# Kernel tuning notes

Measured on AMD Instinct MI355X. Metric: run time of the kernel, lower is better.

## Reference

```python
import jax, jax.numpy as jnp
import numpy as np

NPOINT = 2048
RADII = (0.4, 0.8)
NSAMPLES = (16, 32)
EPS = 1e-5


def _fps(xyz, npoint):
    # iterative farthest point sampling, start at index 0 (matches CUDA kernel)
    B, N, _ = xyz.shape

    def step(carry, _):
        dist, last = carry  # dist [B,N], last [B]
        lx = jnp.take_along_axis(xyz, last[:, None, None], axis=1)  # [B,1,3]
        d = jnp.sum((xyz - lx) ** 2, axis=-1)  # [B,N]
        dist = jnp.minimum(dist, d)
        nxt = jnp.argmax(dist, axis=1).astype(jnp.int32)
        return (dist, nxt), last

    init = (jnp.full((B, N), 1e10, xyz.dtype), jnp.zeros((B,), jnp.int32))
    _, idxs = jax.lax.scan(step, init, None, length=npoint)
    return idxs.T  # [B, npoint]


def _ball_query(radius, nsample, xyz, new_xyz):
    # first-nsample points within radius, in original order; pad with first hit (0 if none)
    N = xyz.shape[1]
    d2 = jnp.sum((new_xyz[:, :, None, :] - xyz[:, None, :, :]) ** 2, axis=-1)  # [B,S,N]
    mask = d2 < radius * radius
    ar = jnp.arange(N, dtype=jnp.int32)
    key = jnp.where(mask, ar, N + ar)  # in-range first, stable original order
    order = jnp.argsort(key, axis=-1)[..., :nsample].astype(jnp.int32)  # [B,S,ns]
    cnt = mask.sum(axis=-1, keepdims=True)  # [B,S,1]
    valid = jnp.arange(nsample) < cnt
    return jnp.where(valid, order, order[..., :1])


def _bn_relu(x):
    # training-mode BatchNorm (gamma=1, beta=0) over all dims but channel (last)
    red = tuple(range(x.ndim - 1))
    mu = x.mean(axis=red, keepdims=True)
    var = x.var(axis=red, keepdims=True)
    return jax.nn.relu((x - mu) * jax.lax.rsqrt(var + EPS))


def _scale(xyz, new_xyz, feats, radius, nsample, ws):
    idx = _ball_query(radius, nsample, xyz, new_xyz)  # [B,S,ns]
    B, S, ns = idx.shape
    flat = idx.reshape(B, S * ns)
    gx = jnp.take_along_axis(xyz, flat[..., None], axis=1).reshape(B, S, ns, 3)
    gx = gx - new_xyz[:, :, None, :]  # relative coords
    gf = jnp.take_along_axis(feats, flat[..., None], axis=1).reshape(B, S, ns, -1)
    h = jnp.concatenate([gx, gf], axis=-1)  # [B,S,ns,3+C]
    for w in ws:
        h = _bn_relu(h @ w)  # pointwise conv (kernel 1) + BN + ReLU
    return h.max(axis=2)  # max-pool over group -> [B,S,Cout]


def setup_inputs() -> dict:
    key = jax.random.key(0)
    ks = jax.random.split(key, 16)
    s = 0.02
    return {
        "xyz": jax.random.normal(ks[0], (8, 8192, 3), jnp.float32),
        "features": jax.random.normal(ks[1], (8, 8192, 64), jnp.float32),
        "w0_0": jax.random.normal(ks[2], (67, 64), jnp.float32) * s,
        "w0_1": jax.random.normal(ks[3], (64, 64), jnp.float32) * s,
        "w0_2": jax.random.normal(ks[4], (64, 128), jnp.float32) * s,
        "w1_0": jax.random.normal(ks[5], (67, 64), jnp.float32) * s,
        "w1_1": jax.random.normal(ks[6], (64, 64), jnp.float32) * s,
        "w1_2": jax.random.normal(ks[7], (64, 128), jnp.float32) * s,
        "agg_w": jax.random.normal(ks[8], (256, 256), jnp.float32) * s,
        "agg_b": jax.random.normal(ks[9], (256,), jnp.float32) * s,
        "conf_w": jax.random.normal(ks[10], (256, 256), jnp.float32) * s,
        "cls_w": jax.random.normal(ks[11], (256, 3), jnp.float32) * s,
        "cls_b": jax.random.normal(ks[12], (3,), jnp.float32) * s,
    }


def reference(xyz, features, w0_0, w0_1, w0_2, w1_0, w1_1, w1_2,
              agg_w, agg_b, conf_w, cls_w, cls_b):
    idx = _fps(xyz, NPOINT)  # [B,S]
    new_xyz = jnp.take_along_axis(xyz, idx[..., None], axis=1)  # [B,S,3]
    f0 = _scale(xyz, new_xyz, features, RADII[0], NSAMPLES[0], (w0_0, w0_1, w0_2))
    f1 = _scale(xyz, new_xyz, features, RADII[1], NSAMPLES[1], (w1_0, w1_1, w1_2))
    h = jnp.concatenate([f0, f1], axis=-1)  # [B,S,256]
    h = _bn_relu(h @ agg_w + agg_b)  # aggregation Linear + BN + ReLU
    c = _bn_relu(h @ conf_w)  # confidence hidden layer
    cls = c @ cls_w + cls_b  # [B,S,num_class]
    return new_xyz, h, cls
```

## Files before the change

### kernel.cpp

```cpp
#include <hip/hip_runtime.h>
#include <cstdint>
#include <cstddef>

constexpr int Bb = 8;
constexpr int Nn = 8192;
constexpr int Ss = 2048;
constexpr int BS = Bb * Ss;

typedef float vfloat2 __attribute__((ext_vector_type(2)));

__global__ __launch_bounds__(1024) void fps_kernel(const float* __restrict__ xyz,
                                                   float* __restrict__ new_xyz) {
  __shared__ float lx[Nn * 3];
  __shared__ int sidx[Ss];
  __shared__ float rv32[2][16];
  __shared__ double rv64[2][16];
  __shared__ int ri[2][16];
  const int b = blockIdx.x;
  const int tid = threadIdx.x;
  const float* xb = xyz + (size_t)b * Nn * 3;
  for (int e = tid; e < Nn * 3; e += 1024) lx[e] = xb[e];
  __syncthreads();
  vfloat2 px2[4], py2[4], pz2[4], df2[4];
  double dist[8];
#pragma unroll
  for (int jj = 0; jj < 4; ++jj) {
    const int p0 = tid + (2 * jj) * 1024, p1 = tid + (2 * jj + 1) * 1024;
    px2[jj] = (vfloat2){lx[p0 * 3 + 0], lx[p1 * 3 + 0]};
    py2[jj] = (vfloat2){lx[p0 * 3 + 1], lx[p1 * 3 + 1]};
    pz2[jj] = (vfloat2){lx[p0 * 3 + 2], lx[p1 * 3 + 2]};
    df2[jj] = (vfloat2){3.0e38f, 3.0e38f};
    dist[2 * jj] = 1e10;
    dist[2 * jj + 1] = 1e10;
  }
  const int lane = tid & 63, wid = tid >> 6;
  int cur = 0;
  double lv = -1.0;
  int li = tid;
  float wv32_c = -1.0f;
  double wv64_c = -1.0;
  int wi_c = 0;
  for (int i = 0; i < Ss; ++i) {
    if (tid == 0) sidx[i] = cur;
    const float cxf = lx[cur * 3 + 0], cyf = lx[cur * 3 + 1], czf = lx[cur * 3 + 2];
    const vfloat2 cx2 = {cxf, cxf}, cy2 = {cyf, cyf}, cz2 = {czf, czf};
    unsigned need = 0;
#pragma unroll
    for (int jj = 0; jj < 4; ++jj) {
      const vfloat2 dx = px2[jj] - cx2;
      const vfloat2 dy = py2[jj] - cy2;
      const vfloat2 dz = pz2[jj] - cz2;
      const vfloat2 d2 = dx * dx + dy * dy + dz * dz;
      need |= (d2.x <= df2[jj].x) ? (1u << (2 * jj)) : 0u;
      need |= (d2.y <= df2[jj].y) ? (1u << (2 * jj + 1)) : 0u;
    }
    bool changed = false;
    if (need) {
#pragma unroll
      for (int j = 0; j < 8; ++j) {
        if (need & (1u << j)) {
          const float pxs = px2[j >> 1][j & 1];
          const float pys = py2[j >> 1][j & 1];
          const float pzs = pz2[j >> 1][j & 1];
          double dx = __dsub_rn((double)pxs, (double)cxf);
          double dy = __dsub_rn((double)pys, (double)cyf);
          double dz = __dsub_rn((double)pzs, (double)czf);
          double d = __dadd_rn(__dadd_rn(__dmul_rn(dx, dx), __dmul_rn(dy, dy)),
                               __dmul_rn(dz, dz));
          if (d < dist[j]) {
            dist[j] = d;
            const float dfn = (float)d * 1.000002f;
            if (j & 1) df2[j >> 1].y = dfn; else df2[j >> 1].x = dfn;
            changed = true;
          }
        }
      }
    }
    const unsigned long long anyb = __ballot(changed);
    if (changed) {
      lv = -1.0;
      li = 0;
#pragma unroll
      for (int j = 0; j < 8; ++j) {
        if (dist[j] > lv) { lv = dist[j]; li = tid + j * 1024; }
      }
    }
    if (anyb) {
      const float lv32 = (float)lv;
      float m32 = lv32;
#pragma unroll
      for (int off = 1; off < 64; off <<= 1) m32 = fmaxf(m32, __shfl_xor(m32, off));
      const unsigned long long em = __ballot(lv32 == m32);
      if (__popcll(em) == 1) {
        const int w = (int)__builtin_ctzll(em);
        wi_c = __shfl(li, w);
        wv64_c = __shfl(lv, w);
        wv32_c = m32;
      } else {
        double bv = lv;
        int bi = li;
#pragma unroll
        for (int off = 1; off < 64; off <<= 1) {
          double ov = __shfl_xor(bv, off);
          int oi = __shfl_xor(bi, off);
          if (ov > bv || (ov == bv && oi < bi)) { bv = ov; bi = oi; }
        }
        wv64_c = bv;
        wi_c = bi;
        wv32_c = (float)bv;
      }
    }
    const int pb = i & 1;
    if (lane == 0) { rv32[pb][wid] = wv32_c; rv64[pb][wid] = wv64_c; ri[pb][wid] = wi_c; }
    __syncthreads();
    const float mine = rv32[pb][lane & 15];
    float g32 = mine;
#pragma unroll
    for (int off = 1; off < 16; off <<= 1) g32 = fmaxf(g32, __shfl_xor(g32, off));
    const unsigned long long bm = __ballot((lane < 16) && (mine == g32));
    if (__popcll(bm) == 1) {
      cur = ri[pb][(int)__builtin_ctzll(bm)];
    } else {
      double gv = -1.0;
      int gi = 0x7fffffff;
      unsigned mm = (unsigned)bm;
      while (mm) {
        const int w = (int)__builtin_ctz(mm);
        mm &= mm - 1;
        const double ov = rv64[pb][w];
        const int oi = ri[pb][w];
        if (ov > gv || (ov == gv && oi < gi)) { gv = ov; gi = oi; }
      }
      cur = gi;
    }
  }
  __syncthreads();
  float* nxb = new_xyz + (size_t)b * Ss * 3;
  for (int e = tid; e < Ss * 3; e += 1024) {
    const int i = e / 3, c = e - i * 3;
    nxb[e] = lx[sidx[i] * 3 + c];
  }
}

__global__ __launch_bounds__(256) void ballq_kernel(const float* __restrict__ xyz,
                                                    const float* __restrict__ nxyz,
                                                    int* __restrict__ idx0,
                                                    int* __restrict__ idx1) {
  const int wid = threadIdx.x >> 6, lane = threadIdx.x & 63;
  const int bs = blockIdx.x * 4 + wid;
  const int b = bs >> 11;
  const float* xb = xyz + (size_t)b * Nn * 3;
  const double cx = (double)nxyz[bs * 3 + 0];
  const double cy = (double)nxyz[bs * 3 + 1];
  const double cz = (double)nxyz[bs * 3 + 2];
  const double R0 = 0.4 * 0.4, R1 = 0.8 * 0.8;
  int cnt0 = 0, cnt1 = 0, first0 = 0, first1 = 0;
  const unsigned long long lmask = (1ull << lane) - 1ull;
  for (int base = 0; base < Nn; base += 64) {
    const int p = base + lane;
    double dx = __dsub_rn((double)xb[p * 3 + 0], cx);
    double dy = __dsub_rn((double)xb[p * 3 + 1], cy);
    double dz = __dsub_rn((double)xb[p * 3 + 2], cz);
    double d2 = __dadd_rn(__dadd_rn(__dmul_rn(dx, dx), __dmul_rn(dy, dy)), __dmul_rn(dz, dz));
    const bool in0 = d2 < R0, in1 = d2 < R1;
    unsigned long long m0 = __ballot(in0);
    unsigned long long m1 = __ballot(in1);
    if (cnt0 < 16 && m0) {
      if (cnt0 == 0) first0 = base + __builtin_ctzll(m0);
      int r = (int)__popcll(m0 & lmask);
      if (in0 && cnt0 + r < 16) idx0[bs * 16 + cnt0 + r] = p;
      cnt0 += (int)__popcll(m0);
    }
    if (cnt1 < 32 && m1) {
      if (cnt1 == 0) first1 = base + __builtin_ctzll(m1);
      int r = (int)__popcll(m1 & lmask);
      if (in1 && cnt1 + r < 32) idx1[bs * 32 + cnt1 + r] = p;
      cnt1 += (int)__popcll(m1);
    }
    if (cnt0 >= 16 && cnt1 >= 32) break;
  }
  const int f0 = cnt0 < 16 ? cnt0 : 16;
  for (int j = f0 + lane; j < 16; j += 64) idx0[bs * 16 + j] = first0;
  const int f1 = cnt1 < 32 ? cnt1 : 32;
  for (int j = f1 + lane; j < 32; j += 64) idx1[bs * 32 + j] = first1;
}

template <int COUT, int KTOT, int MODE, int NS, bool POOL, bool BIAS>
__global__ __launch_bounds__(256) void mlp_gemm(
    const float* __restrict__ xin, const float* __restrict__ xin2,
    const float* __restrict__ bnp, const float* __restrict__ bnp2,
    const float* __restrict__ w, const float* __restrict__ bias,
    const int* __restrict__ gidx, const float* __restrict__ xyz,
    const float* __restrict__ nxyz, const float* __restrict__ feats,
    float* __restrict__ out, float* __restrict__ P) {
  constexpr int KC = (KTOT <= 68) ? KTOT : 32;
  constexpr int NCH = (KTOT + KC - 1) / KC;
  constexpr int TC = COUT / 16;
  constexpr int XPAD = KC + 1;
  constexpr int XSZ = 64 * XPAD;
  constexpr int EPI = (POOL ? 48 : 32) * COUT;
  constexpr int SM = (XSZ + KC * COUT > EPI) ? (XSZ + KC * COUT) : EPI;
  __shared__ float smem[SM];
  float* xS = smem;
  float* wS = smem + XSZ;

  const int tid = threadIdx.x;
  const int cg = tid & 15, rg = tid >> 4;
  const int row0 = blockIdx.x * 64;
  float acc[4][TC];
#pragma unroll
  for (int i = 0; i < 4; ++i)
#pragma unroll
    for (int t = 0; t < TC; ++t) acc[i][t] = 0.f;

  for (int ch = 0; ch < NCH; ++ch) {
    const int k0 = ch * KC;
    if (ch) __syncthreads();
    for (int e = tid; e < 64 * KC; e += 256) {
      const int r = e / KC, kk = e - r * KC;
      const int kg = k0 + kk;
      const int rowg = row0 + r;
      float v;
      if constexpr (MODE == 0) {
        const int bs = rowg / NS;
        const int p = gidx[rowg];
        const int bb = bs >> 11;
        if (kg < 3)
          v = xyz[(bb * Nn + p) * 3 + kg] - nxyz[bs * 3 + kg];
        else
          v = feats[((bb * Nn + p) << 6) + (kg - 3)];
      } else if constexpr (MODE == 1) {
        v = fmaxf((xin[(size_t)rowg * 64 + kg] - bnp[kg]) * bnp[64 + kg], 0.f);
      } else if constexpr (MODE == 2) {
        if (kg < 128)
          v = fmaxf((xin[(size_t)rowg * 128 + kg] - bnp[kg]) * bnp[128 + kg], 0.f);
        else {
          const int k2 = kg - 128;
          v = fmaxf((xin2[(size_t)rowg * 128 + k2] - bnp2[k2]) * bnp2[128 + k2], 0.f);
        }
      } else {
        v = xin[(size_t)rowg * 256 + kg];
      }
      xS[r * XPAD + kk] = v;
    }
    for (int e = tid; e < KC * COUT; e += 256) {
      const int kk = e / COUT, c = e - kk * COUT;
      wS[kk * COUT + c] = w[(size_t)(k0 + kk) * COUT + c];
    }
    __syncthreads();
    for (int kk = 0; kk < KC; ++kk) {
      float xr[4];
#pragma unroll
      for (int i = 0; i < 4; ++i) xr[i] = xS[(rg * 4 + i) * XPAD + kk];
#pragma unroll
      for (int t = 0; t < TC; t += 4) {
        const float4 wv = *(const float4*)&wS[kk * COUT + cg * TC + t];
#pragma unroll
        for (int i = 0; i < 4; ++i) {
          acc[i][t + 0] = fmaf(xr[i], wv.x, acc[i][t + 0]);
          acc[i][t + 1] = fmaf(xr[i], wv.y, acc[i][t + 1]);
          acc[i][t + 2] = fmaf(xr[i], wv.z, acc[i][t + 2]);
          acc[i][t + 3] = fmaf(xr[i], wv.w, acc[i][t + 3]);
        }
      }
    }
  }
  __syncthreads();
  if constexpr (BIAS) {
#pragma unroll
    for (int t = 0; t < TC; ++t) {
      const float bv = bias[cg * TC + t];
#pragma unroll
      for (int i = 0; i < 4; ++i) acc[i][t] += bv;
    }
  }
  float* ssum = smem;
  float* ssq = smem + 16 * COUT;
  float* pbuf = smem + 32 * COUT;
  const int colb = cg * TC;
#pragma unroll
  for (int t = 0; t < TC; ++t) {
    float s = 0.f, q = 0.f, m = -3.4e38f;
#pragma unroll
    for (int i = 0; i < 4; ++i) {
      const float v = acc[i][t];
      s += v;
      q = fmaf(v, v, q);
      m = fmaxf(m, v);
    }
    ssum[rg * COUT + colb + t] = s;
    ssq[rg * COUT + colb + t] = q;
    if constexpr (POOL) pbuf[rg * COUT + colb + t] = m;
  }
  __syncthreads();
  const int gX = gridDim.x;
  for (int c = tid; c < COUT; c += 256) {
    float s = 0.f, q = 0.f;
#pragma unroll
    for (int rr = 0; rr < 16; ++rr) {
      s += ssum[rr * COUT + c];
      q += ssq[rr * COUT + c];
    }
    P[(size_t)c * gX + blockIdx.x] = s;
    P[(size_t)(COUT + c) * gX + blockIdx.x] = q;
  }
  if constexpr (POOL) {
    constexpr int G = 64 / NS, RPG = NS / 4;
    for (int o = tid; o < G * COUT; o += 256) {
      const int g = o / COUT, c = o - g * COUT;
      float m = pbuf[(g * RPG) * COUT + c];
#pragma unroll
      for (int qq = 1; qq < RPG; ++qq) m = fmaxf(m, pbuf[(g * RPG + qq) * COUT + c]);
      out[(size_t)(blockIdx.x * G + g) * COUT + c] = m;
    }
  } else {
#pragma unroll
    for (int i = 0; i < 4; ++i) {
      float* op = out + (size_t)(row0 + rg * 4 + i) * COUT + colb;
#pragma unroll
      for (int t = 0; t < TC; t += 4) {
        *(float4*)(op + t) = make_float4(acc[i][t], acc[i][t + 1], acc[i][t + 2], acc[i][t + 3]);
      }
    }
  }
}

__global__ __launch_bounds__(256) void bn_finalize(const float* __restrict__ P, int gX,
                                                   int M, int C, float* __restrict__ bnp) {
  __shared__ double sh[512];
  const int c = blockIdx.x;
  const int tid = threadIdx.x;
  const float* psum = P + (size_t)c * gX;
  const float* psq = P + (size_t)(C + c) * gX;
  double s = 0, q = 0;
  for (int i = tid; i < gX; i += 256) {
    s += (double)psum[i];
    q += (double)psq[i];
  }
  sh[tid] = s;
  sh[256 + tid] = q;
  __syncthreads();
  for (int off = 128; off; off >>= 1) {
    if (tid < off) {
      sh[tid] += sh[tid + off];
      sh[256 + tid] += sh[256 + tid + off];
    }
    __syncthreads();
  }
  if (tid == 0) {
    const double invM = 1.0 / (double)M;
    const double mu = sh[0] * invM;
    const double var = sh[256] * invM - mu * mu;
    bnp[c] = (float)mu;
    bnp[C + c] = (float)(1.0 / sqrt(var + 1e-5));
  }
}

__global__ __launch_bounds__(256) void h_store_kernel(const float* __restrict__ agg,
                                                      const float* __restrict__ bnp,
                                                      float* __restrict__ hout) {
  const int t = blockIdx.x * 256 + threadIdx.x;
  const int c = t & 255;
  const float v = (agg[t] - bnp[c]) * bnp[256 + c];
  hout[t] = fmaxf(v, 0.f);
}

__global__ __launch_bounds__(256) void cls_kernel(const float* __restrict__ craw,
                                                  const float* __restrict__ bnp,
                                                  const float* __restrict__ clsw,
                                                  const float* __restrict__ clsb,
                                                  float* __restrict__ outc) {
  const int wid = threadIdx.x >> 6, lane = threadIdx.x & 63;
  const int row = blockIdx.x * 4 + wid;
  const float* cr = craw + (size_t)row * 256;
  float a0 = 0.f, a1 = 0.f, a2 = 0.f;
#pragma unroll 4
  for (int k = lane; k < 256; k += 64) {
    float x = fmaxf((cr[k] - bnp[k]) * bnp[256 + k], 0.f);
    a0 = fmaf(x, clsw[k * 3 + 0], a0);
    a1 = fmaf(x, clsw[k * 3 + 1], a1);
    a2 = fmaf(x, clsw[k * 3 + 2], a2);
  }
#pragma unroll
  for (int off = 32; off; off >>= 1) {
    a0 += __shfl_down(a0, off);
    a1 += __shfl_down(a1, off);
    a2 += __shfl_down(a2, off);
  }
  if (lane == 0) {
    outc[row * 3 + 0] = a0 + clsb[0];
    outc[row * 3 + 1] = a1 + clsb[1];
    outc[row * 3 + 2] = a2 + clsb[2];
  }
}

extern "C" void kernel_launch(void* const* d_in, const int* in_sizes, int n_in,
                              void* d_out, int out_size, void* d_ws, size_t ws_size,
                              hipStream_t stream) {
  (void)in_sizes; (void)n_in; (void)out_size; (void)ws_size;
  const float* xyz = (const float*)d_in[0];
  const float* feats = (const float*)d_in[1];
  const float* w00 = (const float*)d_in[2];
  const float* w01 = (const float*)d_in[3];
  const float* w02 = (const float*)d_in[4];
  const float* w10 = (const float*)d_in[5];
  const float* w11 = (const float*)d_in[6];
  const float* w12 = (const float*)d_in[7];
  const float* aggw = (const float*)d_in[8];
  const float* aggb = (const float*)d_in[9];
  const float* confw = (const float*)d_in[10];
  const float* clsw = (const float*)d_in[11];
  const float* clsb = (const float*)d_in[12];

  float* outp = (float*)d_out;
  float* nxyz = outp;
  float* hout = outp + (size_t)BS * 3;
  float* clsout = hout + (size_t)BS * 256;

  char* ws = (char*)d_ws;
  const size_t MB = 1u << 20;
  int* idx0 = (int*)(ws + 0);
  int* idx1 = (int*)(ws + 1 * MB);
  float* bnb = (float*)(ws + 3 * MB);
  float* P = (float*)(ws + 4 * MB);
  float* pool0 = (float*)(ws + 12 * MB);
  float* pool1 = (float*)(ws + 20 * MB);
  float* aggraw = (float*)(ws + 28 * MB);
  float* confraw = (float*)(ws + 44 * MB);
  float* hA = (float*)(ws + 60 * MB);

  fps_kernel<<<Bb, 1024, 0, stream>>>(xyz, nxyz);
  ballq_kernel<<<BS / 4, 256, 0, stream>>>(xyz, nxyz, idx0, idx1);

  mlp_gemm<64, 67, 0, 16, false, false><<<4096, 256, 0, stream>>>(
      nullptr, nullptr, nullptr, nullptr, w00, nullptr, idx0, xyz, nxyz, feats, hA, P);
  bn_finalize<<<64, 256, 0, stream>>>(P, 4096, 262144, 64, bnb + 0);
  mlp_gemm<64, 64, 1, 1, false, false><<<4096, 256, 0, stream>>>(
      hA, nullptr, bnb + 0, nullptr, w01, nullptr, nullptr, nullptr, nullptr, nullptr, hA, P);
  bn_finalize<<<64, 256, 0, stream>>>(P, 4096, 262144, 64, bnb + 128);
  mlp_gemm<128, 64, 1, 16, true, false><<<4096, 256, 0, stream>>>(
      hA, nullptr, bnb + 128, nullptr, w02, nullptr, nullptr, nullptr, nullptr, nullptr, pool0, P);
  bn_finalize<<<128, 256, 0, stream>>>(P, 4096, 262144, 128, bnb + 256);

  mlp_gemm<64, 67, 0, 32, false, false><<<8192, 256, 0, stream>>>(
      nullptr, nullptr, nullptr, nullptr, w10, nullptr, idx1, xyz, nxyz, feats, hA, P);
  bn_finalize<<<64, 256, 0, stream>>>(P, 8192, 524288, 64, bnb + 512);
  mlp_gemm<64, 64, 1, 1, false, false><<<8192, 256, 0, stream>>>(
      hA, nullptr, bnb + 512, nullptr, w11, nullptr, nullptr, nullptr, nullptr, nullptr, hA, P);
  bn_finalize<<<64, 256, 0, stream>>>(P, 8192, 524288, 64, bnb + 640);
  mlp_gemm<128, 64, 1, 32, true, false><<<8192, 256, 0, stream>>>(
      hA, nullptr, bnb + 640, nullptr, w12, nullptr, nullptr, nullptr, nullptr, nullptr, pool1, P);
  bn_finalize<<<128, 256, 0, stream>>>(P, 8192, 524288, 128, bnb + 768);

  mlp_gemm<256, 256, 2, 1, false, true><<<256, 256, 0, stream>>>(
      pool0, pool1, bnb + 256, bnb + 768, aggw, aggb, nullptr, nullptr, nullptr, nullptr, aggraw, P);
  bn_finalize<<<256, 256, 0, stream>>>(P, 256, 16384, 256, bnb + 1024);
  h_store_kernel<<<BS, 256, 0, stream>>>(aggraw, bnb + 1024, hout);

  mlp_gemm<256, 256, 3, 1, false, false><<<256, 256, 0, stream>>>(
      hout, nullptr, nullptr, nullptr, confw, nullptr, nullptr, nullptr, nullptr, nullptr, confraw, P);
  bn_finalize<<<256, 256, 0, stream>>>(P, 256, 16384, 256, bnb + 1536);

  cls_kernel<<<BS / 4, 256, 0, stream>>>(confraw, bnb + 1536, clsw, clsb, clsout);
}
```

Measured before the change: 3.830 ms.

## Spatially sort FPS points per thread and skip distance updates via bounding-sphere test

Points are bucketed into Morton-ordered grid cells with a shared-memory counting sort, so each thread owns 8 spatially nearby points. Each thread keeps a centroid and radius for its points and skips the distance update when the new sample is too far away to lower any of its current minimum distances. This cuts the per-iteration distance arithmetic in the serial FPS loop. The cost is the sort prologue, an extra sortedIdx lookup plus tie-breaking on the smallest original index during the argmax, and shared-memory usage now holding an 8192-entry index array alongside the coordinates.

```diff
diff --git a/kernel.cpp b/kernel.cpp
--- a/kernel.cpp
+++ b/kernel.cpp
@@ -12,66 +12,138 @@
 __global__ __launch_bounds__(1024) void fps_kernel(const float* __restrict__ xyz,
                                                    float* __restrict__ new_xyz) {
   __shared__ float lx[Nn * 3];
-  __shared__ int sidx[Ss];
+  __shared__ int cellbuf[4096];
+  __shared__ int sortedIdx[Nn];
   __shared__ float rv32[2][16];
   __shared__ double rv64[2][16];
   __shared__ int ri[2][16];
+  int* sidx = cellbuf;
+
   const int b = blockIdx.x;
   const int tid = threadIdx.x;
   const float* xb = xyz + (size_t)b * Nn * 3;
   for (int e = tid; e < Nn * 3; e += 1024) lx[e] = xb[e];
-  __syncthreads();
+  for (int e = tid; e < 4096; e += 1024) cellbuf[e] = 0;
+  __syncthreads();
+
+  int mycell[8];
+#pragma unroll
+  for (int j = 0; j < 8; ++j) {
+    const int p = tid + j * 1024;
+    const float x = lx[p * 3 + 0], y = lx[p * 3 + 1], z = lx[p * 3 + 2];
+    int bx = (int)((x + 4.0f) * 2.0f); bx = bx < 0 ? 0 : (bx > 15 ? 15 : bx);
+    int by = (int)((y + 4.0f) * 2.0f); by = by < 0 ? 0 : (by > 15 ? 15 : by);
+    int bz = (int)((z + 4.0f) * 2.0f); bz = bz < 0 ? 0 : (bz > 15 ? 15 : bz);
+    int m = 0;
+#pragma unroll
+    for (int k = 0; k < 4; ++k) {
+      m |= ((bx >> k) & 1) << (3 * k);
+      m |= ((by >> k) & 1) << (3 * k + 1);
+      m |= ((bz >> k) & 1) << (3 * k + 2);
+    }
+    mycell[j] = m;
+    atomicAdd(&cellbuf[m], 1);
+  }
+  __syncthreads();
+  for (int d = 1; d < 4096; d <<= 1) {
+    int v[4];
+#pragma unroll
+    for (int k = 0; k < 4; ++k) {
+      const int e = tid + k * 1024;
+      v[k] = (e >= d) ? cellbuf[e - d] : 0;
+    }
+    __syncthreads();
+#pragma unroll
+    for (int k = 0; k < 4; ++k) cellbuf[tid + k * 1024] += v[k];
+    __syncthreads();
+  }
+  {
+    int v[4];
+#pragma unroll
+    for (int k = 0; k < 4; ++k) {
+      const int e = tid + k * 1024;
+      v[k] = (e == 0) ? 0 : cellbuf[e - 1];
+    }
+    __syncthreads();
+#pragma unroll
+    for (int k = 0; k < 4; ++k) cellbuf[tid + k * 1024] = v[k];
+    __syncthreads();
+  }
+#pragma unroll
+  for (int j = 0; j < 8; ++j) {
+    const int pos = atomicAdd(&cellbuf[mycell[j]], 1);
+    sortedIdx[pos] = tid + j * 1024;
+  }
+  __syncthreads();
+
   vfloat2 px2[4], py2[4], pz2[4], df2[4];
   double dist[8];
-#pragma unroll
-  for (int jj = 0; jj < 4; ++jj) {
-    const int p0 = tid + (2 * jj) * 1024, p1 = tid + (2 * jj + 1) * 1024;
-    px2[jj] = (vfloat2){lx[p0 * 3 + 0], lx[p1 * 3 + 0]};
-    py2[jj] = (vfloat2){lx[p0 * 3 + 1], lx[p1 * 3 + 1]};
-    pz2[jj] = (vfloat2){lx[p0 * 3 + 2], lx[p1 * 3 + 2]};
-    df2[jj] = (vfloat2){3.0e38f, 3.0e38f};
-    dist[2 * jj] = 1e10;
-    dist[2 * jj + 1] = 1e10;
-  }
+  float cenx = 0.f, ceny = 0.f, cenz = 0.f;
+#pragma unroll
+  for (int j = 0; j < 8; ++j) {
+    const int o = sortedIdx[tid * 8 + j];
+    const float x = lx[o * 3 + 0], y = lx[o * 3 + 1], z = lx[o * 3 + 2];
+    if (j & 1) { px2[j >> 1].y = x; py2[j >> 1].y = y; pz2[j >> 1].y = z; }
+    else       { px2[j >> 1].x = x; py2[j >> 1].x = y; pz2[j >> 1].x = z; }
+    cenx += x; ceny += y; cenz += z;
+    dist[j] = 1e10;
+    if (j & 1) df2[j >> 1].y = 3.0e38f; else df2[j >> 1].x = 3.0e38f;
+  }
+  cenx *= 0.125f; ceny *= 0.125f; cenz *= 0.125f;
+  float r2max = 0.f;
+#pragma unroll
+  for (int j = 0; j < 8; ++j) {
+    const float dx = px2[j >> 1][j & 1] - cenx;
+    const float dy = py2[j >> 1][j & 1] - ceny;
+    const float dz = pz2[j >> 1][j & 1] - cenz;
+    r2max = fmaxf(r2max, fmaf(dx, dx, fmaf(dy, dy, dz * dz)));
+  }
+  const float rlane = sqrtf(r2max * (1.0f + 1e-5f)) * (1.0f + 1e-6f);
+  float reach = 3.0e38f;
+
   const int lane = tid & 63, wid = tid >> 6;
   int cur = 0;
   double lv = -1.0;
-  int li = tid;
+  int li = 0x7fffffff;
   float wv32_c = -1.0f;
   double wv64_c = -1.0;
   int wi_c = 0;
   for (int i = 0; i < Ss; ++i) {
     if (tid == 0) sidx[i] = cur;
     const float cxf = lx[cur * 3 + 0], cyf = lx[cur * 3 + 1], czf = lx[cur * 3 + 2];
-    const vfloat2 cx2 = {cxf, cxf}, cy2 = {cyf, cyf}, cz2 = {czf, czf};
-    unsigned need = 0;
-#pragma unroll
-    for (int jj = 0; jj < 4; ++jj) {
-      const vfloat2 dx = px2[jj] - cx2;
-      const vfloat2 dy = py2[jj] - cy2;
-      const vfloat2 dz = pz2[jj] - cz2;
-      const vfloat2 d2 = dx * dx + dy * dy + dz * dz;
-      need |= (d2.x <= df2[jj].x) ? (1u << (2 * jj)) : 0u;
-      need |= (d2.y <= df2[jj].y) ? (1u << (2 * jj + 1)) : 0u;
-    }
+    const float ex = cxf - cenx, ey = cyf - ceny, ez = czf - cenz;
+    const float dc2 = fmaf(ex, ex, fmaf(ey, ey, ez * ez));
     bool changed = false;
-    if (need) {
-#pragma unroll
-      for (int j = 0; j < 8; ++j) {
-        if (need & (1u << j)) {
-          const float pxs = px2[j >> 1][j & 1];
-          const float pys = py2[j >> 1][j & 1];
-          const float pzs = pz2[j >> 1][j & 1];
-          double dx = __dsub_rn((double)pxs, (double)cxf);
-          double dy = __dsub_rn((double)pys, (double)cyf);
-          double dz = __dsub_rn((double)pzs, (double)czf);
-          double d = __dadd_rn(__dadd_rn(__dmul_rn(dx, dx), __dmul_rn(dy, dy)),
-                               __dmul_rn(dz, dz));
-          if (d < dist[j]) {
-            dist[j] = d;
-            const float dfn = (float)d * 1.000002f;
-            if (j & 1) df2[j >> 1].y = dfn; else df2[j >> 1].x = dfn;
-            changed = true;
+    if (!(dc2 * (1.0f - 1e-5f) > reach)) {
+      const vfloat2 cx2 = {cxf, cxf}, cy2 = {cyf, cyf}, cz2 = {czf, czf};
+      unsigned need = 0;
+#pragma unroll
+      for (int jj = 0; jj < 4; ++jj) {
+        const vfloat2 dx = px2[jj] - cx2;
+        const vfloat2 dy = py2[jj] - cy2;
+        const vfloat2 dz = pz2[jj] - cz2;
+        const vfloat2 d2 = dx * dx + dy * dy + dz * dz;
+        need |= (d2.x <= df2[jj].x) ? (1u << (2 * jj)) : 0u;
+        need |= (d2.y <= df2[jj].y) ? (1u << (2 * jj + 1)) : 0u;
+      }
+      if (need) {
+#pragma unroll
+        for (int j = 0; j < 8; ++j) {
+          if (need & (1u << j)) {
+            const float pxs = px2[j >> 1][j & 1];
+            const float pys = py2[j >> 1][j & 1];
+            const float pzs = pz2[j >> 1][j & 1];
+            double dx = __dsub_rn((double)pxs, (double)cxf);
+            double dy = __dsub_rn((double)pys, (double)cyf);
+            double dz = __dsub_rn((double)pzs, (double)czf);
+            double d = __dadd_rn(__dadd_rn(__dmul_rn(dx, dx), __dmul_rn(dy, dy)),
+                                 __dmul_rn(dz, dz));
+            if (d < dist[j]) {
+              dist[j] = d;
+              const float dfn = (float)d * 1.000002f;
+              if (j & 1) df2[j >> 1].y = dfn; else df2[j >> 1].x = dfn;
+              changed = true;
+            }
           }
         }
       }
@@ -79,11 +151,19 @@
     const unsigned long long anyb = __ballot(changed);
     if (changed) {
       lv = -1.0;
-      li = 0;
+      li = 0x7fffffff;
 #pragma unroll
       for (int j = 0; j < 8; ++j) {
-        if (dist[j] > lv) { lv = dist[j]; li = tid + j * 1024; }
-      }
+        const double d = dist[j];
+        if (d > lv) { lv = d; li = sortedIdx[tid * 8 + j]; }
+        else if (d == lv) { const int o = sortedIdx[tid * 8 + j]; li = o < li ? o : li; }
+      }
+      float lmax = df2[0].x;
+      lmax = fmaxf(lmax, df2[0].y);
+#pragma unroll
+      for (int jj = 1; jj < 4; ++jj) { lmax = fmaxf(lmax, df2[jj].x); lmax = fmaxf(lmax, df2[jj].y); }
+      const float s = rlane + sqrtf(lmax) * (1.0f + 1e-6f);
+      reach = s * s * (1.0f + 1e-5f);
     }
     if (anyb) {
       const float lv32 = (float)lv;
```

After: 4.537 ms. 18.5% more time.

## Replace FPS cross-wave argmax with shared-memory atomicMax/atomicMin slots

Applied to the files above, without the earlier changes.

The per-iteration argmax in farthest point sampling now reduces only the value within each wave. It then combines the waves with a 64-bit atomicMax on a shared slot and resolves the index with atomicMin among the lanes that hold the winning value, using double-buffered slots. This removes the float32 pre-reduction, the index shuffles and the serial per-wave tie-break loop. In exchange it adds a second __syncthreads per iteration, and every tied lane contends on the LDS atomic.

```diff
diff --git a/kernel.cpp b/kernel.cpp
--- a/kernel.cpp
+++ b/kernel.cpp
@@ -13,14 +13,18 @@
                                                    float* __restrict__ new_xyz) {
   __shared__ float lx[Nn * 3];
   __shared__ int sidx[Ss];
-  __shared__ float rv32[2][16];
-  __shared__ double rv64[2][16];
-  __shared__ int ri[2][16];
+  __shared__ unsigned long long slotV[2];
+  __shared__ int slotI[2];
   const int b = blockIdx.x;
   const int tid = threadIdx.x;
   const float* xb = xyz + (size_t)b * Nn * 3;
   for (int e = tid; e < Nn * 3; e += 1024) lx[e] = xb[e];
+  if (tid == 0) {
+    slotV[0] = 0ull; slotV[1] = 0ull;
+    slotI[0] = 0x7fffffff; slotI[1] = 0x7fffffff;
+  }
   __syncthreads();
+
   vfloat2 px2[4], py2[4], pz2[4], df2[4];
   double dist[8];
 #pragma unroll
@@ -33,13 +37,11 @@
     dist[2 * jj] = 1e10;
     dist[2 * jj + 1] = 1e10;
   }
-  const int lane = tid & 63, wid = tid >> 6;
+  const int lane = tid & 63;
   int cur = 0;
-  double lv = -1.0;
-  int li = tid;
-  float wv32_c = -1.0f;
-  double wv64_c = -1.0;
-  int wi_c = 0;
+  double lv = 0.0;
+  int li = 0x7fffffff;
+  double wv_c = 0.0;
   for (int i = 0; i < Ss; ++i) {
     if (tid == 0) sidx[i] = cur;
     const float cxf = lx[cur * 3 + 0], cyf = lx[cur * 3 + 1], czf = lx[cur * 3 + 2];
@@ -86,53 +88,22 @@
       }
     }
     if (anyb) {
-      const float lv32 = (float)lv;
-      float m32 = lv32;
-#pragma unroll
-      for (int off = 1; off < 64; off <<= 1) m32 = fmaxf(m32, __shfl_xor(m32, off));
-      const unsigned long long em = __ballot(lv32 == m32);
-      if (__popcll(em) == 1) {
-        const int w = (int)__builtin_ctzll(em);
-        wi_c = __shfl(li, w);
-        wv64_c = __shfl(lv, w);
-        wv32_c = m32;
-      } else {
-        double bv = lv;
-        int bi = li;
-#pragma unroll
-        for (int off = 1; off < 64; off <<= 1) {
-          double ov = __shfl_xor(bv, off);
-          int oi = __shfl_xor(bi, off);
-          if (ov > bv || (ov == bv && oi < bi)) { bv = ov; bi = oi; }
-        }
-        wv64_c = bv;
-        wi_c = bi;
-        wv32_c = (float)bv;
-      }
+      double bv = lv;
+#pragma unroll
+      for (int off = 1; off < 64; off <<= 1) bv = fmax(bv, __shfl_xor(bv, off));
+      wv_c = bv;
     }
     const int pb = i & 1;
-    if (lane == 0) { rv32[pb][wid] = wv32_c; rv64[pb][wid] = wv64_c; ri[pb][wid] = wi_c; }
+    if (lane == 0) atomicMax(&slotV[pb], __double_as_longlong(wv_c));
     __syncthreads();
-    const float mine = rv32[pb][lane & 15];
-    float g32 = mine;
-#pragma unroll
-    for (int off = 1; off < 16; off <<= 1) g32 = fmaxf(g32, __shfl_xor(g32, off));
-    const unsigned long long bm = __ballot((lane < 16) && (mine == g32));
-    if (__popcll(bm) == 1) {
-      cur = ri[pb][(int)__builtin_ctzll(bm)];
-    } else {
-      double gv = -1.0;
-      int gi = 0x7fffffff;
-      unsigned mm = (unsigned)bm;
-      while (mm) {
-        const int w = (int)__builtin_ctz(mm);
-        mm &= mm - 1;
-        const double ov = rv64[pb][w];
-        const int oi = ri[pb][w];
-        if (ov > gv || (ov == gv && oi < gi)) { gv = ov; gi = oi; }
-      }
-      cur = gi;
-    }
+    const double W = __longlong_as_double((long long)slotV[pb]);
+    if (lv == W) atomicMin(&slotI[pb], li);
+    if (tid == 0) {
+      slotV[pb ^ 1] = 0ull;
+      slotI[pb ^ 1] = 0x7fffffff;
+    }
+    __syncthreads();
+    cur = slotI[pb];
   }
   __syncthreads();
   float* nxb = new_xyz + (size_t)b * Ss * 3;
```

New measurement: 3.855 ms. No clear change (+0.6%).
